# Performance work log

Hardware: AMD Instinct MI355X
Metric: run time of the kernel (lower is better)

## Reference

```python
import jax, jax.numpy as jnp
import numpy as np

EPS = 1e-12  # layer_norm_eps

def gelu_bert(x):
    return 0.5 * x * (1.0 + jax.lax.erf(x / jnp.sqrt(2.0).astype(x.dtype)))

def sym_normalize(A):
    # D^{-1/2} A D^{-1/2} via outer-product scaling (algebraic form of diag matmuls)
    d = A.sum(-1)                      # [B,N] row sums
    dinv = jnp.power(d, -0.5)
    return A * dinv[..., :, None] * dinv[..., None, :]

def layernorm(x, g, b):
    mu = x.mean(-1, keepdims=True)
    var = ((x - mu) ** 2).mean(-1, keepdims=True)
    return (x - mu) * jax.lax.rsqrt(var + EPS) * g + b

def gcn(x, adj, w1, w2):
    x = jax.nn.relu(jnp.matmul(adj, x @ w1))   # [B,N,I]
    x = jax.nn.relu(jnp.matmul(adj, x @ w2))   # [B,N,H]
    return x

def setup_inputs() -> dict:
    B, N, H, I = 8, 1024, 768, 3072
    key = jax.random.key(0)
    ks = jax.random.split(key, 20)
    s = 0.02
    inp = {
        'nodes': jax.random.normal(ks[0], (B, N, H), jnp.float32),
        'graphs': jax.random.uniform(ks[1], (B, 2, N, N), jnp.float32),
        'gcn1_w1': jax.random.normal(ks[2], (H, I), jnp.float32) * s,
        'gcn1_w2': jax.random.normal(ks[3], (I, H), jnp.float32) * s,
        'gcn2_w1': jax.random.normal(ks[4], (H, I), jnp.float32) * s,
        'gcn2_w2': jax.random.normal(ks[5], (I, H), jnp.float32) * s,
        'exp1_w': jax.random.normal(ks[6], (H, I), jnp.float32) * s,
        'exp1_b': jnp.zeros((I,), jnp.float32),
        'col1_w': jax.random.normal(ks[7], (I, H), jnp.float32) * s,
        'col1_b': jnp.zeros((H,), jnp.float32),
        'exp2_w': jax.random.normal(ks[8], (H, I), jnp.float32) * s,
        'exp2_b': jnp.zeros((I,), jnp.float32),
        'col2_w': jax.random.normal(ks[9], (I, H), jnp.float32) * s,
        'col2_b': jnp.zeros((H,), jnp.float32),
        'gate_w': jax.random.normal(ks[10], (4 * H, H), jnp.float32) * s,
        'gate_b': jnp.zeros((H,), jnp.float32),
        'ln1_g': jnp.ones((H,), jnp.float32),
        'ln1_b': jnp.zeros((H,), jnp.float32),
        'ln2_g': jnp.ones((H,), jnp.float32),
        'ln2_b': jnp.zeros((H,), jnp.float32),
    }
    return inp

def reference(nodes, graphs, gcn1_w1, gcn1_w2, gcn2_w1, gcn2_w2,
              exp1_w, exp1_b, col1_w, col1_b, exp2_w, exp2_b, col2_w, col2_b,
              gate_w, gate_b, ln1_g, ln1_b, ln2_g, ln2_b):
    adj1 = sym_normalize(graphs[:, 0])   # [B,N,N]
    adj2 = sym_normalize(graphs[:, 1])
    g1 = gcn(nodes, adj1, gcn1_w1, gcn1_w2)  # [B,N,H]
    g2 = gcn(nodes, adj2, gcn2_w1, gcn2_w2)
    # FFN + residual + LN (dropout = identity at eval)
    g1 = gelu_bert(g1 @ exp1_w + exp1_b) @ col1_w + col1_b
    g1 = layernorm(nodes + g1, ln1_g, ln1_b)
    g2 = gelu_bert(g2 @ exp2_w + exp2_b) @ col2_w + col2_b
    g2 = layernorm(nodes + g2, ln2_g, ln2_b)
    gate_in = jnp.concatenate((g1, g2, g1 + g2, g1 - g2), axis=2)  # [B,N,4H]
    gate = jax.nn.sigmoid(gate_in @ gate_w + gate_b)
    return gate * g1 + (1.0 - gate) * g2
```

## Files before the change

### kernel.cpp

```cpp
#include <hip/hip_runtime.h>
#include <hip/hip_bf16.h>

typedef __bf16 b8v __attribute__((ext_vector_type(8)));
typedef float  f4v __attribute__((ext_vector_type(4)));
typedef unsigned long long ull;

#define AS3(p)  ((__attribute__((address_space(3))) void*)(p))
#define AS1C(p) ((const __attribute__((address_space(1))) void*)(p))
#define MFMA16(a, b, c) __builtin_amdgcn_mfma_f32_16x16x32_bf16((a), (b), (c), 0, 0, 0)

template<int EPI, int SWZ>
__global__ __launch_bounds__(512, 2) void gemm256(
    const __hip_bfloat16* __restrict__ A,  long long sA,
    const __hip_bfloat16* __restrict__ Bt, long long sBg, long long sBb, int ldB,
    __hip_bfloat16* __restrict__ C, long long sC, int ldC,
    const float* __restrict__ bias0, const float* __restrict__ bias1, int K)
{
  int bx, by, bz;
  if constexpr (SWZ) {
    const int logical = ((int)blockIdx.x & 7) * 24 + ((int)blockIdx.x >> 3);
    bz = logical / 12;
    const int r = logical - bz * 12;
    by = r >> 2; bx = r & 3;
  } else {
    bx = blockIdx.x; by = blockIdx.y; bz = blockIdx.z;
  }
  A  += (long long)bz * sA;
  Bt += (long long)(bz >> 3) * sBg + (long long)(bz & 7) * sBb;
  const float* __restrict__ bias = (bz & 1) ? bias1 : bias0;

  __shared__ __hip_bfloat16 As[2][2][8192];
  __shared__ __hip_bfloat16 Bs[2][2][8192];

  const int tid  = threadIdx.x;
  const int lane = tid & 63;
  const int wave = tid >> 6;
  const int wr = wave >> 2;
  const int wc = wave & 3;
  const int lm = lane & 15;
  const int kq = lane >> 4;

  const long long m0 = (long long)bx * 256;
  const long long n0 = (long long)by * 256;

  const int sr  = tid >> 3;
  const int sc  = tid & 7;
  const int gch = sc ^ (sr & 7);
  const int ldsE = tid * 8;

  auto stageA = [&](int d, int h, int kt) {
    const __hip_bfloat16* s0 = A + (m0 + h * 128 + sr) * (long long)K + (long long)kt * 64 + gch * 8;
    __builtin_amdgcn_global_load_lds(AS1C(s0),            AS3(&As[d][h][ldsE]),        16, 0, 0);
    __builtin_amdgcn_global_load_lds(AS1C(s0 + 64LL * K), AS3(&As[d][h][4096 + ldsE]), 16, 0, 0);
  };
  auto stageB = [&](int d, int h, int kt) {
    const __hip_bfloat16* s0 = Bt + (n0 + h * 128 + sr) * (long long)ldB + (long long)kt * 64 + gch * 8;
    __builtin_amdgcn_global_load_lds(AS1C(s0),              AS3(&Bs[d][h][ldsE]),        16, 0, 0);
    __builtin_amdgcn_global_load_lds(AS1C(s0 + 64LL * ldB), AS3(&Bs[d][h][4096 + ldsE]), 16, 0, 0);
  };

  const int NT = K >> 6;
  stageA(0, 0, 0); stageA(0, 1, 0); stageB(0, 0, 0); stageB(0, 1, 0);
  stageA(1, 0, 1);
  asm volatile("s_waitcnt vmcnt(2)" ::: "memory");
  __builtin_amdgcn_s_barrier();

  f4v acc[8][4];
  const f4v fz = {0.0f, 0.0f, 0.0f, 0.0f};
#pragma unroll
  for (int i = 0; i < 8; i++)
#pragma unroll
    for (int j = 0; j < 4; j++) acc[i][j] = fz;

  const int rb  = lm * 64;
  const int cs0 = ((kq)     ^ (lm & 7)) * 8;
  const int cs1 = ((4 + kq) ^ (lm & 7)) * 8;

  for (int kt = 0; kt < NT; ++kt) {
    const int d = kt & 1, dn = d ^ 1;
    const __hip_bfloat16* Ab = &As[d][wr][0];
    const __hip_bfloat16* Bb = &Bs[d][wc >> 1][(wc & 1) * 4096];
    const bool st1 = (kt + 1 < NT);
    b8v afL[8], afH[8], bfL[4], bfH[4];

#pragma unroll
    for (int f = 0; f < 4; f++) {
      afL[f * 2]     = *(const b8v*)(Ab + f * 1024 + rb + cs0);
      afL[f * 2 + 1] = *(const b8v*)(Ab + f * 1024 + rb + cs1);
    }
#pragma unroll
    for (int f = 0; f < 2; f++) {
      bfL[f * 2]     = *(const b8v*)(Bb + f * 1024 + rb + cs0);
      bfL[f * 2 + 1] = *(const b8v*)(Bb + f * 1024 + rb + cs1);
    }
    if (st1) stageA(dn, 1, kt + 1);
    __builtin_amdgcn_s_barrier();
    asm volatile("s_waitcnt lgkmcnt(0)" ::: "memory");
    __builtin_amdgcn_sched_barrier(0);
    __builtin_amdgcn_s_setprio(1);
#pragma unroll
    for (int i = 0; i < 4; i++)
#pragma unroll
      for (int j = 0; j < 2; j++) acc[i][j] = MFMA16(bfL[j * 2], afL[i * 2], acc[i][j]);
#pragma unroll
    for (int i = 0; i < 4; i++)
#pragma unroll
      for (int j = 0; j < 2; j++) acc[i][j] = MFMA16(bfL[j * 2 + 1], afL[i * 2 + 1], acc[i][j]);
    __builtin_amdgcn_s_setprio(0);
    __builtin_amdgcn_s_barrier();

#pragma unroll
    for (int f = 0; f < 2; f++) {
      bfH[f * 2]     = *(const b8v*)(Bb + (2 + f) * 1024 + rb + cs0);
      bfH[f * 2 + 1] = *(const b8v*)(Bb + (2 + f) * 1024 + rb + cs1);
    }
    if (st1) stageB(dn, 0, kt + 1);
    __builtin_amdgcn_s_barrier();
    asm volatile("s_waitcnt lgkmcnt(0)" ::: "memory");
    __builtin_amdgcn_sched_barrier(0);
    __builtin_amdgcn_s_setprio(1);
#pragma unroll
    for (int i = 0; i < 4; i++)
#pragma unroll
      for (int j = 0; j < 2; j++) acc[i][2 + j] = MFMA16(bfH[j * 2], afL[i * 2], acc[i][2 + j]);
#pragma unroll
    for (int i = 0; i < 4; i++)
#pragma unroll
      for (int j = 0; j < 2; j++) acc[i][2 + j] = MFMA16(bfH[j * 2 + 1], afL[i * 2 + 1], acc[i][2 + j]);
    __builtin_amdgcn_s_setprio(0);
    __builtin_amdgcn_s_barrier();

#pragma unroll
    for (int f = 0; f < 4; f++) {
      afH[f * 2]     = *(const b8v*)(Ab + (4 + f) * 1024 + rb + cs0);
      afH[f * 2 + 1] = *(const b8v*)(Ab + (4 + f) * 1024 + rb + cs1);
    }
    if (st1) stageB(dn, 1, kt + 1);
    __builtin_amdgcn_s_barrier();
    asm volatile("s_waitcnt lgkmcnt(0)" ::: "memory");
    __builtin_amdgcn_sched_barrier(0);
    __builtin_amdgcn_s_setprio(1);
#pragma unroll
    for (int i = 0; i < 4; i++)
#pragma unroll
      for (int j = 0; j < 2; j++) acc[4 + i][j] = MFMA16(bfL[j * 2], afH[i * 2], acc[4 + i][j]);
#pragma unroll
    for (int i = 0; i < 4; i++)
#pragma unroll
      for (int j = 0; j < 2; j++) acc[4 + i][j] = MFMA16(bfL[j * 2 + 1], afH[i * 2 + 1], acc[4 + i][j]);
    __builtin_amdgcn_s_setprio(0);
    __builtin_amdgcn_s_barrier();

    if (kt + 2 < NT) stageA(d, 0, kt + 2);
    __builtin_amdgcn_s_setprio(1);
#pragma unroll
    for (int i = 0; i < 4; i++)
#pragma unroll
      for (int j = 0; j < 2; j++) acc[4 + i][2 + j] = MFMA16(bfH[j * 2], afH[i * 2], acc[4 + i][2 + j]);
#pragma unroll
    for (int i = 0; i < 4; i++)
#pragma unroll
      for (int j = 0; j < 2; j++) acc[4 + i][2 + j] = MFMA16(bfH[j * 2 + 1], afH[i * 2 + 1], acc[4 + i][2 + j]);
    __builtin_amdgcn_s_setprio(0);
    if (kt + 2 < NT) asm volatile("s_waitcnt vmcnt(2)" ::: "memory");
    else             asm volatile("s_waitcnt vmcnt(0)" ::: "memory");
    __builtin_amdgcn_s_barrier();
  }

#pragma unroll
  for (int i = 0; i < 8; i++) {
    const long long row = m0 + wr * 128 + i * 16 + lm;
#pragma unroll
    for (int j = 0; j < 4; j++) {
      const int colb = (int)n0 + wc * 64 + j * 16 + kq * 4;
      float v[4];
#pragma unroll
      for (int rg = 0; rg < 4; rg++) v[rg] = acc[i][j][rg];
      if constexpr (EPI == 1) {
#pragma unroll
        for (int rg = 0; rg < 4; rg++) v[rg] = fmaxf(v[rg], 0.0f);
      }
      if constexpr (EPI == 2) {
        const float4 b4 = *(const float4*)(bias + colb);
        const float* bb = (const float*)&b4;
#pragma unroll
        for (int rg = 0; rg < 4; rg++) {
          float x = v[rg] + bb[rg];
          v[rg] = 0.5f * x * (1.0f + erff(x * 0.70710678118654752f));
        }
      }
      union { __hip_bfloat16 h[4]; ull u; } P;
#pragma unroll
      for (int rg = 0; rg < 4; rg++) P.h[rg] = __float2bfloat16(v[rg]);
      *(ull*)(C + (long long)bz * sC + row * (long long)ldC + colb) = P.u;
    }
  }
}

template<int EPI, int OBF, int ORIENT, int MP>
__global__ __launch_bounds__(256) void gemm_bt(
    const __hip_bfloat16* __restrict__ A,  long long sA,
    const __hip_bfloat16* __restrict__ Bt, long long sBg, long long sBb, int ldB,
    void* __restrict__ Cv, long long sC, int ldC,
    const float* __restrict__ bias0, const float* __restrict__ bias1,
    const __hip_bfloat16* __restrict__ gcat, int K)
{
  const int bz = blockIdx.z;
  A  += (long long)bz * sA;
  Bt += (long long)(bz >> 3) * sBg + (long long)(bz & 7) * sBb;
  const float* __restrict__ bias = (bz & 1) ? bias1 : bias0;

  __shared__ __hip_bfloat16 As[128 * 32];
  __shared__ __hip_bfloat16 Bs[128 * 32];

  const int tid  = threadIdx.x;
  const int lane = tid & 63;
  const int wave = tid >> 6;

  const long long mBase = (long long)blockIdx.x * (MP * 128);
  const long long n0    = (long long)blockIdx.y * 128;

  const int r  = tid >> 2;
  const int kc = (tid & 3) ^ ((r >> 2) & 3);
  const __hip_bfloat16* aRow = A  + (mBase + r) * (long long)K   + kc * 8;
  const __hip_bfloat16* bRow = Bt + (n0 + r)    * (long long)ldB + kc * 8;

  const int wm = (wave & 1) * 64;
  const int wn = (wave >> 1) * 64;
  const int lm = lane & 15;
  const int kq = lane >> 4;

  const int sw   = (lm >> 2) & 3;
  const int aOff = (wm + lm) * 32 + (kq ^ sw) * 8;
  const int bOff = (wn + lm) * 32 + (kq ^ sw) * 8;

  auto stage = [&](long long aoff, int k0) {
    const __hip_bfloat16* a = aRow + aoff + k0;
    const __hip_bfloat16* b = bRow + k0;
    __builtin_amdgcn_global_load_lds(AS1C(a),              AS3(As + tid * 8),        16, 0, 0);
    __builtin_amdgcn_global_load_lds(AS1C(a + 64LL * K),   AS3(As + 2048 + tid * 8), 16, 0, 0);
    __builtin_amdgcn_global_load_lds(AS1C(b),              AS3(Bs + tid * 8),        16, 0, 0);
    __builtin_amdgcn_global_load_lds(AS1C(b + 64LL * ldB), AS3(Bs + 2048 + tid * 8), 16, 0, 0);
  };

  stage(0, 0);

  const f4v fzero = {0.0f, 0.0f, 0.0f, 0.0f};
  char* Cb = (char*)Cv;

  for (int p = 0; p < MP; ++p) {
    const long long aoff = (long long)p * 128 * K;

    f4v acc[4][4];
#pragma unroll
    for (int i = 0; i < 4; i++)
#pragma unroll
      for (int j = 0; j < 4; j++) acc[i][j] = fzero;

    for (int k0 = 0; k0 < K; k0 += 32) {
      __syncthreads();

      b8v af[4], bf[4];
#pragma unroll
      for (int i = 0; i < 4; i++) af[i] = *(const b8v*)(As + aOff + i * 16 * 32);
#pragma unroll
      for (int j = 0; j < 4; j++) bf[j] = *(const b8v*)(Bs + bOff + j * 16 * 32);

      __syncthreads();

      if (k0 + 32 < K)            stage(aoff, k0 + 32);
      else if (MP > 1 && p + 1 < MP) stage(aoff + 128LL * K, 0);

#pragma unroll
      for (int i = 0; i < 4; i++)
#pragma unroll
        for (int j = 0; j < 4; j++) {
          if constexpr (ORIENT == 0)
            acc[i][j] = __builtin_amdgcn_mfma_f32_16x16x32_bf16(bf[j], af[i], acc[i][j], 0, 0, 0);
          else
            acc[i][j] = __builtin_amdgcn_mfma_f32_16x16x32_bf16(af[i], bf[j], acc[i][j], 0, 0, 0);
        }
    }

    const long long m0 = mBase + (long long)p * 128;
#pragma unroll
    for (int i = 0; i < 4; i++) {
#pragma unroll
      for (int j = 0; j < 4; j++) {
        float v[4];
#pragma unroll
        for (int rg = 0; rg < 4; rg++) v[rg] = acc[i][j][rg];

        if constexpr (ORIENT == 0) {
          const long long row  = m0 + wm + i * 16 + lm;
          const int       colb = (int)n0 + wn + j * 16 + kq * 4;
          if constexpr (EPI == 1) {
#pragma unroll
            for (int rg = 0; rg < 4; rg++) v[rg] = fmaxf(v[rg], 0.0f);
          }
          if constexpr (EPI == 2) {
            const float4 b4 = *(const float4*)(bias + colb);
            const float* bb = (const float*)&b4;
#pragma unroll
            for (int rg = 0; rg < 4; rg++) {
              float x = v[rg] + bb[rg];
              v[rg] = 0.5f * x * (1.0f + erff(x * 0.70710678118654752f));
            }
          }
          const long long base = bz * sC + row * (long long)ldC + colb;
          if constexpr (EPI == 3) {
            const float4 b4 = *(const float4*)(bias0 + colb);
            const float* bb = (const float*)&b4;
            union { __hip_bfloat16 h[4]; ull u; } g1, g2;
            g1.u = *(const ull*)(gcat + row * 1536 + colb);
            g2.u = *(const ull*)(gcat + row * 1536 + 768 + colb);
            float o[4];
#pragma unroll
            for (int rg = 0; rg < 4; rg++) {
              const float s = 1.0f / (1.0f + expf(-(v[rg] + bb[rg])));
              o[rg] = s * __bfloat162float(g1.h[rg]) +
                      (1.0f - s) * __bfloat162float(g2.h[rg]);
            }
            *(float4*)(Cb + base * 4) = *(const float4*)o;
          } else if constexpr (OBF) {
            union { __hip_bfloat16 h[4]; ull u; } P;
#pragma unroll
            for (int rg = 0; rg < 4; rg++) P.h[rg] = __float2bfloat16(v[rg]);
            *(ull*)(Cb + base * 2) = P.u;
          } else {
            *(float4*)(Cb + base * 4) = *(const float4*)v;
          }
        } else {
          const long long crow = n0 + wn + j * 16 + lm;
          const long long mb   = m0 + wm + i * 16 + kq * 4;
          if constexpr (EPI == 1) {
#pragma unroll
            for (int rg = 0; rg < 4; rg++) v[rg] = fmaxf(v[rg], 0.0f);
          }
          const long long base = bz * sC + crow * (long long)ldC + mb;
          if constexpr (OBF) {
            union { __hip_bfloat16 h[4]; ull u; } P;
#pragma unroll
            for (int rg = 0; rg < 4; rg++) P.h[rg] = __float2bfloat16(v[rg]);
            *(ull*)(Cb + base * 2) = P.u;
          } else {
            *(float4*)(Cb + base * 4) = *(const float4*)v;
          }
        }
      }
    }
  }
}

__global__ __launch_bounds__(256) void rowsum_dinv(const float* __restrict__ g,
                                                   float* __restrict__ dinv)
{
  const int wave = threadIdx.x >> 6, lane = threadIdx.x & 63;
  const long long row = (long long)blockIdx.x * 4 + wave;
  const float4* p = (const float4*)(g + row * 1024);
  float s = 0.0f;
#pragma unroll
  for (int k = 0; k < 4; k++) {
    float4 v = p[lane + k * 64];
    s += v.x + v.y + v.z + v.w;
  }
#pragma unroll
  for (int o = 32; o > 0; o >>= 1) s += __shfl_down(s, o);
  if (lane == 0) dinv[row] = 1.0f / sqrtf(s);
}

__global__ __launch_bounds__(256) void scale_adj(const float* __restrict__ g,
                                                 const float* __restrict__ dinv,
                                                 __hip_bfloat16* __restrict__ out)
{
  const long long t = (long long)blockIdx.x * 256 + threadIdx.x;
  const long long e = t * 4;
  const int m = (int)(e >> 20);
  const int i = (int)((e >> 10) & 1023);
  const int j = (int)(e & 1023);
  const float4 v  = *(const float4*)(g + e);
  const float  di = dinv[m * 1024 + i];
  const float4 dj = *(const float4*)(dinv + m * 1024 + j);
  const int om = (m & 1) * 8 + (m >> 1);
  union { __hip_bfloat16 h[4]; ull u; } r;
  r.h[0] = __float2bfloat16(v.x * di * dj.x);
  r.h[1] = __float2bfloat16(v.y * di * dj.y);
  r.h[2] = __float2bfloat16(v.z * di * dj.z);
  r.h[3] = __float2bfloat16(v.w * di * dj.w);
  *(ull*)(out + ((long long)om << 20) + (long long)i * 1024 + j) = r.u;
}

template<typename TIN>
__global__ void transpose_conv(const TIN* __restrict__ in, __hip_bfloat16* __restrict__ out,
                               int R, int C, long long sIn, long long sOut)
{
  __shared__ __hip_bfloat16 tile[32][33];
  in  += (long long)blockIdx.z * sIn;
  out += (long long)blockIdx.z * sOut;
  const int c0 = blockIdx.x * 32, r0 = blockIdx.y * 32;
  const int tx = threadIdx.x, ty = threadIdx.y;
#pragma unroll
  for (int i = 0; i < 32; i += 8)
    tile[ty + i][tx] = __float2bfloat16((float)in[(long long)(r0 + ty + i) * C + c0 + tx]);
  __syncthreads();
#pragma unroll
  for (int i = 0; i < 32; i += 8)
    out[(long long)(c0 + ty + i) * R + r0 + tx] = tile[tx][ty + i];
}

__global__ __launch_bounds__(256) void ln_residual2(
    const float* __restrict__ nodes, const __hip_bfloat16* __restrict__ V,
    const float* __restrict__ colb0, const float* __restrict__ colb1,
    const float* __restrict__ lng0,  const float* __restrict__ lng1,
    const float* __restrict__ lnb0,  const float* __restrict__ lnb1,
    __hip_bfloat16* __restrict__ gcat)
{
  const long long row = blockIdx.x;
  const int g = (int)(row >> 13);
  const long long rr = row & 8191;
  const float* __restrict__ colb = g ? colb1 : colb0;
  const float* __restrict__ lng  = g ? lng1  : lng0;
  const float* __restrict__ lnb  = g ? lnb1  : lnb0;
  const int t = threadIdx.x;
  const long long nbase = rr * 768;
  const long long vbase = row * 768;
  float x[3]; float s = 0.0f, ss = 0.0f;
#pragma unroll
  for (int i = 0; i < 3; i++) {
    const int c = t + i * 256;
    const float v = nodes[nbase + c] + __bfloat162float(V[vbase + c]) + colb[c];
    x[i] = v; s += v; ss += v * v;
  }
  __shared__ float red[8];
#pragma unroll
  for (int o = 32; o > 0; o >>= 1) { s += __shfl_down(s, o); ss += __shfl_down(ss, o); }
  const int wave = t >> 6, lane = t & 63;
  if (lane == 0) { red[wave] = s; red[4 + wave] = ss; }
  __syncthreads();
  if (t == 0) {
    red[0] = red[0] + red[1] + red[2] + red[3];
    red[4] = red[4] + red[5] + red[6] + red[7];
  }
  __syncthreads();
  const float mu  = red[0] * (1.0f / 768.0f);
  float var = red[4] * (1.0f / 768.0f) - mu * mu;
  var = fmaxf(var, 0.0f);
  const float rs = rsqrtf(var + 1e-12f);
#pragma unroll
  for (int i = 0; i < 3; i++) {
    const int c = t + i * 256;
    const float y = (x[i] - mu) * rs * lng[c] + lnb[c];
    gcat[rr * 1536 + g * 768 + c] = __float2bfloat16(y);
  }
}

__global__ __launch_bounds__(256) void build_wefft(const float* __restrict__ gw,
                                                   __hip_bfloat16* __restrict__ wt)
{
  const int idx = blockIdx.x * 256 + threadIdx.x;
  const int n = idx / 1536, k = idx % 1536;
  float v;
  if (k < 768) v = gw[k * 768 + n] + gw[(1536 + k) * 768 + n] + gw[(2304 + k) * 768 + n];
  else {
    const int kk = k - 768;
    v = gw[(768 + kk) * 768 + n] + gw[(1536 + kk) * 768 + n] - gw[(2304 + kk) * 768 + n];
  }
  wt[idx] = __float2bfloat16(v);
}

extern "C" void kernel_launch(void* const* d_in, const int* in_sizes, int n_in,
                              void* d_out, int out_size, void* d_ws, size_t ws_size,
                              hipStream_t stream)
{
  const float* nodes  = (const float*)d_in[0];
  const float* graphs = (const float*)d_in[1];
  const float* gcn_w1[2] = { (const float*)d_in[2], (const float*)d_in[4] };
  const float* gcn_w2[2] = { (const float*)d_in[3], (const float*)d_in[5] };
  const float* exp_w[2]  = { (const float*)d_in[6],  (const float*)d_in[10] };
  const float* exp_b[2]  = { (const float*)d_in[7],  (const float*)d_in[11] };
  const float* col_w[2]  = { (const float*)d_in[8],  (const float*)d_in[12] };
  const float* col_b[2]  = { (const float*)d_in[9],  (const float*)d_in[13] };
  const float* gate_w = (const float*)d_in[14];
  const float* gate_b = (const float*)d_in[15];
  const float* ln_g[2] = { (const float*)d_in[16], (const float*)d_in[18] };
  const float* ln_b[2] = { (const float*)d_in[17], (const float*)d_in[19] };
  float* out = (float*)d_out;

  char* w = (char*)d_ws;
  auto alloc = [&](size_t bytes) { char* p = w; w += (bytes + 255) & ~(size_t)255; return p; };
  float*          dinv   = (float*)alloc(16384ULL * 4);
  char*           regA   = alloc(16ULL * 1024 * 1024 * 2);
  __hip_bfloat16* adj2   = (__hip_bfloat16*)regA;
  __hip_bfloat16* Gcat   = (__hip_bfloat16*)regA;
  __hip_bfloat16* wefft  = (__hip_bfloat16*)alloc(768ULL * 1536 * 2);
  __hip_bfloat16* bufA2  = (__hip_bfloat16*)alloc(16ULL * 1024 * 768 * 2);
  char*           regD   = alloc(16ULL * 1024 * 768 * 2);
  __hip_bfloat16* Xt     = (__hip_bfloat16*)regD;
  __hip_bfloat16* bufB2  = (__hip_bfloat16*)regD;
  __hip_bfloat16* X12    = (__hip_bfloat16*)alloc(2ULL * 8192 * 3072 * 2);
  __hip_bfloat16* wgt1   = (__hip_bfloat16*)alloc(2ULL * 3072 * 768 * 2);
  __hip_bfloat16* wgt2   = (__hip_bfloat16*)alloc(2ULL * 768 * 3072 * 2);

  const long long sW1 = 3072LL * 768;
  const long long sW2 = 768LL * 3072;
  const long long sNM = 1024LL * 768;
  const long long sBig = 8192LL * 3072;

  rowsum_dinv<<<4096, 256, 0, stream>>>(graphs, dinv);
  transpose_conv<float><<<dim3(24, 32, 8), dim3(32, 8), 0, stream>>>(
      nodes, Xt, 1024, 768, 1024LL * 768, 768LL * 1024);
  build_wefft<<<4608, 256, 0, stream>>>(gate_w, wefft);
  scale_adj<<<16384, 256, 0, stream>>>(graphs, dinv, adj2);
  for (int g = 0; g < 2; g++) {
    transpose_conv<float><<<dim3(96, 24, 1), dim3(32, 8), 0, stream>>>(
        gcn_w1[g], wgt1 + g * sW1, 768, 3072, 0, 0);
    transpose_conv<float><<<dim3(24, 96, 1), dim3(32, 8), 0, stream>>>(
        gcn_w2[g], wgt2 + g * sW2, 3072, 768, 0, 0);
  }

  gemm256<0, 1><<<192, 512, 0, stream>>>(
      adj2, 1LL << 20, Xt, 0, sNM, 1024, bufA2, sNM, 768,
      nullptr, nullptr, 1024);
  gemm256<1, 0><<<dim3(32, 12, 2), 512, 0, stream>>>(
      bufA2, 8192LL * 768, wgt1, 0, sW1, 768, X12, sBig, 3072,
      nullptr, nullptr, 768);
  gemm256<0, 0><<<dim3(3, 32, 2), 512, 0, stream>>>(
      wgt2, sW2, X12, 0, sBig, 3072, bufA2, 768LL * 8192, 8192,
      nullptr, nullptr, 3072);
  for (int g = 0; g < 2; g++) {
    transpose_conv<float><<<dim3(96, 24, 1), dim3(32, 8), 0, stream>>>(
        exp_w[g], wgt1 + g * sW1, 768, 3072, 0, 0);
    transpose_conv<float><<<dim3(24, 96, 1), dim3(32, 8), 0, stream>>>(
        col_w[g], wgt2 + g * sW2, 3072, 768, 0, 0);
  }
  gemm256<1, 1><<<192, 512, 0, stream>>>(
      adj2, 1LL << 20, bufA2, 768LL * 8192, 1024, 8192, bufB2, sNM, 768,
      nullptr, nullptr, 1024);
  gemm256<2, 0><<<dim3(32, 12, 2), 512, 0, stream>>>(
      bufB2, 8192LL * 768, wgt1, 0, sW1, 768, X12, sBig, 3072,
      exp_b[0], exp_b[1], 768);
  gemm256<0, 0><<<dim3(32, 3, 2), 512, 0, stream>>>(
      X12, sBig, wgt2, 0, sW2, 3072, bufA2, 8192LL * 768, 768,
      nullptr, nullptr, 3072);
  ln_residual2<<<16384, 256, 0, stream>>>(
      nodes, bufA2, col_b[0], col_b[1], ln_g[0], ln_g[1], ln_b[0], ln_b[1], Gcat);
  gemm_bt<3, 0, 0, 1><<<dim3(64, 6, 1), 256, 0, stream>>>(
      Gcat, 0, wefft, 0, 0, 1536, out, 0, 768,
      gate_b, nullptr, Gcat, 1536);
}
```

Baseline: 798.3 us.

## Collapse four-phase GEMM k-loop into single fragment load and MFMA block

Replaces the four-phase ping-pong schedule, which interleaved partial LDS fragment loads, staged global-to-LDS copies, barriers and setprio around quarter MFMA blocks, with one phase. Each k-step now loads all A and B fragments up front, issues all next-tile staging, does one barrier, then runs all 64 MFMAs. This cuts per-iteration barriers and waitcnt stalls and raises the live fragment register count. It loses the fine-grained overlap of LDS reads with MFMA work and the cross-wave priority scheduling.

```diff
diff --git a/kernel.cpp b/kernel.cpp
--- a/kernel.cpp
+++ b/kernel.cpp
@@ -64,6 +64,7 @@
   stageA(1, 0, 1);
   asm volatile("s_waitcnt vmcnt(2)" ::: "memory");
   __builtin_amdgcn_s_barrier();
+  __builtin_amdgcn_sched_barrier(0);
 
   f4v acc[8][4];
   const f4v fz = {0.0f, 0.0f, 0.0f, 0.0f};
@@ -81,90 +82,37 @@
     const __hip_bfloat16* Ab = &As[d][wr][0];
     const __hip_bfloat16* Bb = &Bs[d][wc >> 1][(wc & 1) * 4096];
     const bool st1 = (kt + 1 < NT);
-    b8v afL[8], afH[8], bfL[4], bfH[4];
-
+    b8v af[16], bf[8];
+
+#pragma unroll
+    for (int f = 0; f < 8; f++) {
+      af[f * 2]     = *(const b8v*)(Ab + f * 1024 + rb + cs0);
+      af[f * 2 + 1] = *(const b8v*)(Ab + f * 1024 + rb + cs1);
+    }
 #pragma unroll
     for (int f = 0; f < 4; f++) {
-      afL[f * 2]     = *(const b8v*)(Ab + f * 1024 + rb + cs0);
-      afL[f * 2 + 1] = *(const b8v*)(Ab + f * 1024 + rb + cs1);
+      bf[f * 2]     = *(const b8v*)(Bb + f * 1024 + rb + cs0);
+      bf[f * 2 + 1] = *(const b8v*)(Bb + f * 1024 + rb + cs1);
     }
-#pragma unroll
-    for (int f = 0; f < 2; f++) {
-      bfL[f * 2]     = *(const b8v*)(Bb + f * 1024 + rb + cs0);
-      bfL[f * 2 + 1] = *(const b8v*)(Bb + f * 1024 + rb + cs1);
-    }
-    if (st1) stageA(dn, 1, kt + 1);
+    if (st1) { stageA(dn, 1, kt + 1); stageB(dn, 0, kt + 1); stageB(dn, 1, kt + 1); }
+
+    __builtin_amdgcn_sched_barrier(0);
     __builtin_amdgcn_s_barrier();
-    asm volatile("s_waitcnt lgkmcnt(0)" ::: "memory");
     __builtin_amdgcn_sched_barrier(0);
-    __builtin_amdgcn_s_setprio(1);
-#pragma unroll
-    for (int i = 0; i < 4; i++)
-#pragma unroll
-      for (int j = 0; j < 2; j++) acc[i][j] = MFMA16(bfL[j * 2], afL[i * 2], acc[i][j]);
-#pragma unroll
-    for (int i = 0; i < 4; i++)
-#pragma unroll
-      for (int j = 0; j < 2; j++) acc[i][j] = MFMA16(bfL[j * 2 + 1], afL[i * 2 + 1], acc[i][j]);
-    __builtin_amdgcn_s_setprio(0);
-    __builtin_amdgcn_s_barrier();
-
-#pragma unroll
-    for (int f = 0; f < 2; f++) {
-      bfH[f * 2]     = *(const b8v*)(Bb + (2 + f) * 1024 + rb + cs0);
-      bfH[f * 2 + 1] = *(const b8v*)(Bb + (2 + f) * 1024 + rb + cs1);
-    }
-    if (st1) stageB(dn, 0, kt + 1);
-    __builtin_amdgcn_s_barrier();
-    asm volatile("s_waitcnt lgkmcnt(0)" ::: "memory");
-    __builtin_amdgcn_sched_barrier(0);
-    __builtin_amdgcn_s_setprio(1);
-#pragma unroll
-    for (int i = 0; i < 4; i++)
-#pragma unroll
-      for (int j = 0; j < 2; j++) acc[i][2 + j] = MFMA16(bfH[j * 2], afL[i * 2], acc[i][2 + j]);
-#pragma unroll
-    for (int i = 0; i < 4; i++)
-#pragma unroll
-      for (int j = 0; j < 2; j++) acc[i][2 + j] = MFMA16(bfH[j * 2 + 1], afL[i * 2 + 1], acc[i][2 + j]);
-    __builtin_amdgcn_s_setprio(0);
-    __builtin_amdgcn_s_barrier();
-
-#pragma unroll
-    for (int f = 0; f < 4; f++) {
-      afH[f * 2]     = *(const b8v*)(Ab + (4 + f) * 1024 + rb + cs0);
-      afH[f * 2 + 1] = *(const b8v*)(Ab + (4 + f) * 1024 + rb + cs1);
-    }
-    if (st1) stageB(dn, 1, kt + 1);
-    __builtin_amdgcn_s_barrier();
-    asm volatile("s_waitcnt lgkmcnt(0)" ::: "memory");
-    __builtin_amdgcn_sched_barrier(0);
-    __builtin_amdgcn_s_setprio(1);
-#pragma unroll
-    for (int i = 0; i < 4; i++)
-#pragma unroll
-      for (int j = 0; j < 2; j++) acc[4 + i][j] = MFMA16(bfL[j * 2], afH[i * 2], acc[4 + i][j]);
-#pragma unroll
-    for (int i = 0; i < 4; i++)
-#pragma unroll
-      for (int j = 0; j < 2; j++) acc[4 + i][j] = MFMA16(bfL[j * 2 + 1], afH[i * 2 + 1], acc[4 + i][j]);
-    __builtin_amdgcn_s_setprio(0);
-    __builtin_amdgcn_s_barrier();
-
     if (kt + 2 < NT) stageA(d, 0, kt + 2);
-    __builtin_amdgcn_s_setprio(1);
-#pragma unroll
-    for (int i = 0; i < 4; i++)
-#pragma unroll
-      for (int j = 0; j < 2; j++) acc[4 + i][2 + j] = MFMA16(bfH[j * 2], afH[i * 2], acc[4 + i][2 + j]);
-#pragma unroll
-    for (int i = 0; i < 4; i++)
-#pragma unroll
-      for (int j = 0; j < 2; j++) acc[4 + i][2 + j] = MFMA16(bfH[j * 2 + 1], afH[i * 2 + 1], acc[4 + i][2 + j]);
-    __builtin_amdgcn_s_setprio(0);
+
+#pragma unroll
+    for (int i = 0; i < 8; i++)
+#pragma unroll
+      for (int j = 0; j < 4; j++) {
+        acc[i][j] = MFMA16(bf[j * 2],     af[i * 2],     acc[i][j]);
+        acc[i][j] = MFMA16(bf[j * 2 + 1], af[i * 2 + 1], acc[i][j]);
+      }
+
     if (kt + 2 < NT) asm volatile("s_waitcnt vmcnt(2)" ::: "memory");
     else             asm volatile("s_waitcnt vmcnt(0)" ::: "memory");
     __builtin_amdgcn_s_barrier();
+    __builtin_amdgcn_sched_barrier(0);
   }
 
 #pragma unroll
```

Result: no change. 798.3 us (+0.0%).
